# Kernel optimization log

Measured on AMD Instinct MI355X. Metric: run time of the kernel, lower is better.

## Reference

```python
import jax, jax.numpy as jnp
import numpy as np

B, S, E, H = 8, 1024, 1024, 16
D = E // H  # head dimension = 64


def setup_inputs() -> dict:
    key = jax.random.key(0)
    ks = jax.random.split(key, 9)
    sc = 1.0 / np.sqrt(E)
    return {
        "q": jax.random.normal(ks[0], (B, S, E), dtype=jnp.float32),
        "Wq_w": jax.random.normal(ks[1], (E, E), dtype=jnp.float32) * sc,
        "Wq_b": jax.random.normal(ks[2], (E,), dtype=jnp.float32) * 0.01,
        "Wk_w": jax.random.normal(ks[3], (E, E), dtype=jnp.float32) * sc,
        "Wk_b": jax.random.normal(ks[4], (E,), dtype=jnp.float32) * 0.01,
        "Wv_w": jax.random.normal(ks[5], (E, E), dtype=jnp.float32) * sc,
        "Wv_b": jax.random.normal(ks[6], (E,), dtype=jnp.float32) * 0.01,
        "Wo_w": jax.random.normal(ks[7], (E, E), dtype=jnp.float32) * sc,
        "Wo_b": jax.random.normal(ks[8], (E,), dtype=jnp.float32) * 0.01,
    }


def reference(q, Wq_w, Wq_b, Wk_w, Wk_b, Wv_w, Wv_b, Wo_w, Wo_b):
    # Linear projections (torch Linear: x @ W.T + b)
    Q = q @ Wq_w.T + Wq_b
    K = q @ Wk_w.T + Wk_b  # self-attention: k = v = q
    V = q @ Wv_w.T + Wv_b
    # [B, S, E] -> [B, H, S, D]
    Q = Q.reshape(B, S, H, D).transpose(0, 2, 1, 3)
    K = K.reshape(B, S, H, D).transpose(0, 2, 1, 3)
    V = V.reshape(B, S, H, D).transpose(0, 2, 1, 3)
    # Scores [B, H, S, S], scaled by sqrt(head_dim)
    scores = jnp.einsum('bhqd,bhkd->bhqk', Q, K) / jnp.sqrt(jnp.float32(D))
    attn = jax.nn.softmax(scores, axis=-1)
    # dropout p=0.0 (eval mode) -> identity
    out = jnp.einsum('bhqk,bhkd->bhqd', attn, V)
    out = out.transpose(0, 2, 1, 3).reshape(B, S, E)
    out = out @ Wo_w.T + Wo_b
    return out, attn
```

## Files before the change

### kernel.cpp

```cpp
#include <hip/hip_runtime.h>

using bf16x8 = __attribute__((ext_vector_type(8))) __bf16;
using f32x4  = __attribute__((ext_vector_type(4))) float;

#define NE 1024
#define C1E 0.18033688011112042f
#define C2E -11.541560327111707f

__device__ __forceinline__ unsigned short f2b(float f) {
    unsigned u = __builtin_bit_cast(unsigned, f);
    u = (u + 0x7FFFu + ((u >> 16) & 1u)) >> 16;
    return (unsigned short)u;
}

typedef __attribute__((address_space(1))) const void gvoid_t;
typedef __attribute__((address_space(3))) void lvoid_t;


__device__ __forceinline__ void stage128(const unsigned short* gbase, char* lds, int tid)
{
    const int w = tid >> 6, l = tid & 63;
    #pragma unroll
    for (int i = 0; i < 4; ++i) {
        int grp = i * 4 + w;
        int row = grp * 8 + (l >> 3);
        int srcb = ((l & 7) * 16) ^ ((l >> 3) << 4);
        const char* g = (const char*)(gbase + (size_t)row * NE) + srcb;
        __builtin_amdgcn_global_load_lds((gvoid_t*)g, (lvoid_t*)(lds + grp * 1024), 16, 0, 0);
    }
}

__device__ __forceinline__ void stage64x128(const unsigned short* gbase, char* lds, int tid)
{
    const int w = tid >> 6, l = tid & 63;
    #pragma unroll
    for (int i = 0; i < 2; ++i) {
        int grp = i * 4 + w;
        int row = grp * 8 + (l >> 3);
        int srcb = ((l & 7) * 16) ^ ((l >> 3) << 4);
        const char* g = (const char*)(gbase + (size_t)row * NE) + srcb;
        __builtin_amdgcn_global_load_lds((gvoid_t*)g, (lvoid_t*)(lds + grp * 1024), 16, 0, 0);
    }
}

__device__ __forceinline__ void stage64x256(const unsigned short* gbase, char* lds, int tid)
{
    const int w = tid >> 6, l = tid & 63;
    #pragma unroll
    for (int i = 0; i < 4; ++i) {
        int row0 = i * 16 + w * 4;
        int row = row0 + (l >> 4);
        int srcb = ((l & 15) * 16) ^ ((row & 7) << 4);
        const char* g = (const char*)(gbase + (size_t)row * 1024) + srcb;
        __builtin_amdgcn_global_load_lds((gvoid_t*)g, (lvoid_t*)(lds + row0 * 256), 16, 0, 0);
    }
}

__global__ __launch_bounds__(256)
void conv_bf16(const float* __restrict__ src, unsigned short* __restrict__ dst)
{
    size_t i = ((size_t)blockIdx.x * 256 + threadIdx.x) * 8;
    float4 a0 = *(const float4*)(src + i);
    float4 a1 = *(const float4*)(src + i + 4);
    uint4 p;
    p.x = f2b(a0.x) | ((unsigned)f2b(a0.y) << 16);
    p.y = f2b(a0.z) | ((unsigned)f2b(a0.w) << 16);
    p.z = f2b(a1.x) | ((unsigned)f2b(a1.y) << 16);
    p.w = f2b(a1.z) | ((unsigned)f2b(a1.w) << 16);
    *(uint4*)(dst + i) = p;
}

__global__ __launch_bounds__(256)
void conv_all(const float* __restrict__ q, const float* __restrict__ w0,
              const float* __restrict__ w1, const float* __restrict__ w2,
              unsigned short* __restrict__ qd, unsigned short* __restrict__ d0,
              unsigned short* __restrict__ d1, unsigned short* __restrict__ d2)
{
    int bid = blockIdx.x;
    const float* s; unsigned short* d; size_t off;
    if (bid < 4096) { s = q; d = qd; off = (size_t)bid * 2048; }
    else {
        int seg = (bid - 4096) >> 9, r = (bid - 4096) & 511;
        s = seg == 0 ? w0 : (seg == 1 ? w1 : w2);
        d = seg == 0 ? d0 : (seg == 1 ? d1 : d2);
        off = (size_t)r * 2048;
    }
    size_t i = off + threadIdx.x * 8;
    float4 a0 = *(const float4*)(s + i);
    float4 a1 = *(const float4*)(s + i + 4);
    uint4 p;
    p.x = f2b(a0.x) | ((unsigned)f2b(a0.y) << 16);
    p.y = f2b(a0.z) | ((unsigned)f2b(a0.w) << 16);
    p.z = f2b(a1.x) | ((unsigned)f2b(a1.y) << 16);
    p.w = f2b(a1.z) | ((unsigned)f2b(a1.w) << 16);
    *(uint4*)(d + i) = p;
}

__global__ __launch_bounds__(256, 2)
void qkv_proj(const unsigned short* __restrict__ A,
              const unsigned short* __restrict__ Wq, const unsigned short* __restrict__ Wk,
              const unsigned short* __restrict__ Wv,
              const float* __restrict__ bq, const float* __restrict__ bk,
              const float* __restrict__ bv,
              unsigned short* __restrict__ Qo, unsigned short* __restrict__ Ko,
              unsigned short* __restrict__ Vo)
{
    __shared__ char Asm[16384];
    __shared__ char Bsm[3][8192];
    const int tid  = threadIdx.x;
    const int lane = tid & 63;
    const int w    = tid >> 6;
    const int swz = (blockIdx.x & 7) * 128 + (blockIdx.x >> 3);
    const int rowbase = (swz >> 4) * 128;
    const int colbase = (swz & 15) * 64;
    f32x4 acc[3][2][4] = {};

    for (int kt = 0; kt < 16; ++kt) {
        __syncthreads();
        stage128(A + (size_t)rowbase * NE + kt * 64, Asm, tid);
        stage64x128(Wq + (size_t)colbase * NE + kt * 64, Bsm[0], tid);
        stage64x128(Wk + (size_t)colbase * NE + kt * 64, Bsm[1], tid);
        stage64x128(Wv + (size_t)colbase * NE + kt * 64, Bsm[2], tid);
        __syncthreads();
        #pragma unroll
        for (int ks = 0; ks < 2; ++ks) {
            const int kb = ks * 64 + (lane >> 4) * 16;
            bf16x8 af[2], bf[3][4];
            #pragma unroll
            for (int m = 0; m < 2; ++m) {
                int row = w * 32 + m * 16 + (lane & 15);
                af[m] = *(const bf16x8*)(Asm + ((row * 128 + kb) ^ ((row & 7) << 4)));
            }
            #pragma unroll
            for (int j = 0; j < 3; ++j)
                #pragma unroll
                for (int n = 0; n < 4; ++n) {
                    int row = n * 16 + (lane & 15);
                    bf[j][n] = *(const bf16x8*)(Bsm[j] + ((row * 128 + kb) ^ ((row & 7) << 4)));
                }
            #pragma unroll
            for (int j = 0; j < 3; ++j)
                #pragma unroll
                for (int m = 0; m < 2; ++m)
                    #pragma unroll
                    for (int n = 0; n < 4; ++n)
                        acc[j][m][n] = __builtin_amdgcn_mfma_f32_16x16x32_bf16(af[m], bf[j][n], acc[j][m][n], 0, 0, 0);
        }
    }

    #pragma unroll
    for (int m = 0; m < 2; ++m)
        #pragma unroll
        for (int n = 0; n < 4; ++n) {
            int col = colbase + n * 16 + (lane & 15);
            float bvq = bq[col], bvk = bk[col], bvv = bv[col];
            #pragma unroll
            for (int r = 0; r < 4; ++r) {
                int row = rowbase + w * 32 + m * 16 + (lane >> 4) * 4 + r;
                Qo[(size_t)row * NE + col] = f2b(acc[0][m][n][r] + bvq);
                Ko[(size_t)row * NE + col] = f2b(acc[1][m][n][r] + bvk);
                int b = row >> 10, s = row & 1023, h = col >> 6, d = col & 63;
                Vo[((size_t)((b * 16 + h) * 64 + d) << 10) + s] = f2b(acc[2][m][n][r] + bvv);
            }
        }
}

__global__ __launch_bounds__(256)
void proj_o(const unsigned short* __restrict__ A, const unsigned short* __restrict__ W,
            const float* __restrict__ bias, float* __restrict__ outp)
{
    __shared__ char Asm[16384], Bsm[16384];
    const int tid  = threadIdx.x;
    const int lane = tid & 63;
    const int wid  = tid >> 6;
    const int wr = wid >> 1, wc = wid & 1;
    const int swz = (blockIdx.x & 7) * 64 + (blockIdx.x >> 3);
    const int rowbase = (swz >> 3) * 128;
    const int colbase = (swz & 7) * 128;
    f32x4 acc[4][4] = {};

    for (int kt = 0; kt < 16; ++kt) {
        __syncthreads();
        stage128(A + (size_t)rowbase * NE + kt * 64, Asm, tid);
        stage128(W + (size_t)colbase * NE + kt * 64, Bsm, tid);
        __syncthreads();
        #pragma unroll
        for (int ks = 0; ks < 2; ++ks) {
            const int kb = ks * 64 + (lane >> 4) * 16;
            bf16x8 af[4], bf[4];
            #pragma unroll
            for (int m = 0; m < 4; ++m) {
                int row = wr * 64 + m * 16 + (lane & 15);
                af[m] = *(const bf16x8*)(Asm + ((row * 128 + kb) ^ ((row & 7) << 4)));
            }
            #pragma unroll
            for (int n = 0; n < 4; ++n) {
                int row = wc * 64 + n * 16 + (lane & 15);
                bf[n] = *(const bf16x8*)(Bsm + ((row * 128 + kb) ^ ((row & 7) << 4)));
            }
            #pragma unroll
            for (int m = 0; m < 4; ++m)
                #pragma unroll
                for (int n = 0; n < 4; ++n)
                    acc[m][n] = __builtin_amdgcn_mfma_f32_16x16x32_bf16(af[m], bf[n], acc[m][n], 0, 0, 0);
        }
    }

    #pragma unroll
    for (int m = 0; m < 4; ++m)
        #pragma unroll
        for (int n = 0; n < 4; ++n) {
            int col = colbase + wc * 64 + n * 16 + (lane & 15);
            float bv = bias[col];
            #pragma unroll
            for (int r = 0; r < 4; ++r) {
                int row = rowbase + wr * 64 + m * 16 + (lane >> 4) * 4 + r;
                outp[(size_t)row * NE + col] = acc[m][n][r] + bv;
            }
        }
}

__global__ __launch_bounds__(256, 2)
void fused_attn(const unsigned short* __restrict__ Q,
                const unsigned short* __restrict__ K,
                const unsigned short* __restrict__ VT,
                float* __restrict__ attn, unsigned short* __restrict__ Og)
{
    __shared__ char Ksm[16384];
    __shared__ char Vsm[16384];
    __shared__ char Psm[32768];
    __shared__ float rs4[4][128];
    __shared__ float lt[128];
    const int tid  = threadIdx.x;
    const int lane = tid & 63;
    const int w    = tid >> 6;
    const int swzb = (blockIdx.x & 7) * 128 + (blockIdx.x >> 3);
    const int bh = swzb >> 3, qt = swzb & 7;
    const int b = bh >> 4, h = bh & 15;
    const unsigned short* Qg = Q  + (size_t)(b * 1024 + qt * 128) * 1024 + h * 64;
    const unsigned short* Kg = K  + (size_t)(b * 1024) * 1024 + h * 64;
    const unsigned short* Vg = VT + (size_t)bh * 64 * 1024;

    stage128(Qg, Psm, tid);
    __syncthreads();
    bf16x8 qf[2][8];
    #pragma unroll
    for (int ks = 0; ks < 2; ++ks) {
        const int kb = ks * 64 + (lane >> 4) * 16;
        #pragma unroll
        for (int n = 0; n < 8; ++n) {
            int row = n * 16 + (lane & 15);
            qf[ks][n] = *(const bf16x8*)(Psm + ((row * 128 + kb) ^ ((row & 7) << 4)));
        }
    }
    stage128(Kg, Ksm, tid);

    float rs_p[8] = {0.f, 0.f, 0.f, 0.f, 0.f, 0.f, 0.f, 0.f};
    for (int kt = 0; kt < 8; ++kt) {
        __syncthreads();
        f32x4 sa[2][8] = {};
        __builtin_amdgcn_s_setprio(1);
        #pragma unroll
        for (int ks = 0; ks < 2; ++ks) {
            const int kb = ks * 64 + (lane >> 4) * 16;
            bf16x8 kf[2];
            #pragma unroll
            for (int m = 0; m < 2; ++m) {
                int row = w * 32 + m * 16 + (lane & 15);
                kf[m] = *(const bf16x8*)(Ksm + ((row * 128 + kb) ^ ((row & 7) << 4)));
            }
            #pragma unroll
            for (int m = 0; m < 2; ++m)
                #pragma unroll
                for (int n = 0; n < 8; ++n)
                    sa[m][n] = __builtin_amdgcn_mfma_f32_16x16x32_bf16(kf[m], qf[ks][n], sa[m][n], 0, 0, 0);
        }
        __builtin_amdgcn_s_setprio(0);
        __syncthreads();
        if (kt < 7) stage128(Kg + (size_t)((kt + 1) * 128) * 1024, Ksm, tid);
        #pragma unroll
        for (int n = 0; n < 8; ++n)
            #pragma unroll
            for (int m = 0; m < 2; ++m)
                #pragma unroll
                for (int r = 0; r < 4; ++r)
                    rs_p[n] += exp2f(fmaf(sa[m][n][r], C1E, C2E));
    }
    #pragma unroll
    for (int n = 0; n < 8; ++n) {
        rs_p[n] += __shfl_xor(rs_p[n], 16);
        rs_p[n] += __shfl_xor(rs_p[n], 32);
    }
    if (lane < 16) {
        #pragma unroll
        for (int n = 0; n < 8; ++n) rs4[w][n * 16 + lane] = rs_p[n];
    }
    __syncthreads();
    if (tid < 128) {
        float l = rs4[0][tid] + rs4[1][tid] + rs4[2][tid] + rs4[3][tid];
        lt[tid] = C2E - __log2f(l);
    }
    stage128(Kg, Ksm, tid);

    f32x4 oa[2][4] = {};
    float* attnq = attn + ((size_t)bh * 1024 + qt * 128) * 1024;
    for (int kt = 0; kt < 8; ++kt) {
        __syncthreads();
        stage64x256(Vg + kt * 128, Vsm, tid);
        f32x4 sa[2][8] = {};
        __builtin_amdgcn_s_setprio(1);
        #pragma unroll
        for (int ks = 0; ks < 2; ++ks) {
            const int kb = ks * 64 + (lane >> 4) * 16;
            bf16x8 kf[2];
            #pragma unroll
            for (int m = 0; m < 2; ++m) {
                int row = w * 32 + m * 16 + (lane & 15);
                kf[m] = *(const bf16x8*)(Ksm + ((row * 128 + kb) ^ ((row & 7) << 4)));
            }
            #pragma unroll
            for (int m = 0; m < 2; ++m)
                #pragma unroll
                for (int n = 0; n < 8; ++n)
                    sa[m][n] = __builtin_amdgcn_mfma_f32_16x16x32_bf16(kf[m], qf[ks][n], sa[m][n], 0, 0, 0);
        }
        __builtin_amdgcn_s_setprio(0);
        #pragma unroll
        for (int n = 0; n < 8; ++n) {
            int q = n * 16 + (lane & 15);
            float ltq = lt[q];
            #pragma unroll
            for (int m = 0; m < 2; ++m) {
                int k0 = w * 32 + m * 16 + (lane >> 4) * 4;
                float4 p4;
                p4.x = exp2f(fmaf(sa[m][n][0], C1E, ltq));
                p4.y = exp2f(fmaf(sa[m][n][1], C1E, ltq));
                p4.z = exp2f(fmaf(sa[m][n][2], C1E, ltq));
                p4.w = exp2f(fmaf(sa[m][n][3], C1E, ltq));
                *(float4*)(attnq + (size_t)q * 1024 + kt * 128 + k0) = p4;
                uint2 pk;
                pk.x = f2b(p4.x) | ((unsigned)f2b(p4.y) << 16);
                pk.y = f2b(p4.z) | ((unsigned)f2b(p4.w) << 16);
                *(uint2*)(Psm + ((q * 256 + k0 * 2) ^ ((q & 7) << 4))) = pk;
            }
        }
        __syncthreads();
        if (kt < 7) stage128(Kg + (size_t)((kt + 1) * 128) * 1024, Ksm, tid);
        __builtin_amdgcn_s_setprio(1);
        #pragma unroll
        for (int ks = 0; ks < 4; ++ks) {
            const int kb = ks * 64 + (lane >> 4) * 16;
            bf16x8 pa[2], vb[4];
            #pragma unroll
            for (int m2 = 0; m2 < 2; ++m2) {
                int row = w * 32 + m2 * 16 + (lane & 15);
                pa[m2] = *(const bf16x8*)(Psm + ((row * 256 + kb) ^ ((row & 7) << 4)));
            }
            #pragma unroll
            for (int n2 = 0; n2 < 4; ++n2) {
                int d = n2 * 16 + (lane & 15);
                vb[n2] = *(const bf16x8*)(Vsm + d * 256 + (kb ^ ((d & 7) << 4)));
            }
            #pragma unroll
            for (int m2 = 0; m2 < 2; ++m2)
                #pragma unroll
                for (int n2 = 0; n2 < 4; ++n2)
                    oa[m2][n2] = __builtin_amdgcn_mfma_f32_16x16x32_bf16(pa[m2], vb[n2], oa[m2][n2], 0, 0, 0);
        }
        __builtin_amdgcn_s_setprio(0);
    }
    unsigned short* Ob = Og + (size_t)(b * 1024 + qt * 128) * 1024 + h * 64;
    #pragma unroll
    for (int m2 = 0; m2 < 2; ++m2)
        #pragma unroll
        for (int n2 = 0; n2 < 4; ++n2) {
            int d = n2 * 16 + (lane & 15);
            #pragma unroll
            for (int r = 0; r < 4; ++r) {
                int qrow = w * 32 + m2 * 16 + (lane >> 4) * 4 + r;
                Ob[(size_t)qrow * 1024 + d] = f2b(oa[m2][n2][r]);
            }
        }
}

extern "C" void kernel_launch(void* const* d_in, const int* in_sizes, int n_in,
                              void* d_out, int out_size, void* d_ws, size_t ws_size,
                              hipStream_t stream) {
    (void)in_sizes; (void)n_in; (void)out_size; (void)ws_size;
    const float* q    = (const float*)d_in[0];
    const float* Wq_w = (const float*)d_in[1];
    const float* Wq_b = (const float*)d_in[2];
    const float* Wk_w = (const float*)d_in[3];
    const float* Wk_b = (const float*)d_in[4];
    const float* Wv_w = (const float*)d_in[5];
    const float* Wv_b = (const float*)d_in[6];
    const float* Wo_w = (const float*)d_in[7];
    const float* Wo_b = (const float*)d_in[8];

    char* ws = (char*)d_ws;
    unsigned short* Qws  = (unsigned short*)(ws);
    unsigned short* Kws  = (unsigned short*)(ws + (16u << 20));
    unsigned short* VTws = (unsigned short*)(ws + (32u << 20));

    float* outp  = (float*)d_out;
    float* attnp = outp + 8388608;

    char* scr = (char*)attnp;
    unsigned short* qbf = (unsigned short*)scr;
    unsigned short* wqb = (unsigned short*)(scr + (16u << 20));
    unsigned short* wkb = (unsigned short*)(scr + (18u << 20));
    unsigned short* wvb = (unsigned short*)(scr + (20u << 20));

    dim3 blk(256);
    conv_all<<<dim3(4096 + 3 * 512), blk, 0, stream>>>(q, Wq_w, Wk_w, Wv_w, qbf, wqb, wkb, wvb);
    qkv_proj<<<dim3(1024), blk, 0, stream>>>(qbf, wqb, wkb, wvb, Wq_b, Wk_b, Wv_b, Qws, Kws, VTws);
    fused_attn<<<dim3(1024), blk, 0, stream>>>(Qws, Kws, VTws, attnp, Qws);
    conv_bf16<<<dim3(512), blk, 0, stream>>>(Wo_w, Kws);
    proj_o<<<dim3(512), blk, 0, stream>>>(Qws, Kws, Wo_b, outp);
}
```

Before: 278.0 us.

## Halve P tile LDS, double-buffer K in row-sum pass, raise occupancy to 3

Shrinks the P staging buffer from 32KB to 16KB by writing and consuming the probability tile in two 64-key halves, with extra barriers between halves. This allows launch bounds of 3 blocks per CU instead of 2. The first row-sum pass now double-buffers K tiles between Ksm and the freed Psm, removing one barrier per iteration and overlapping loads with MFMA work. It also swaps the manual bf16 rounding for native casts. The risks are more register pressure under the tighter bound and more synchronisation in the PV loop.

```diff
diff --git a/kernel.cpp b/kernel.cpp
--- a/kernel.cpp
+++ b/kernel.cpp
@@ -1,6 +1,7 @@
 #include <hip/hip_runtime.h>
 
 using bf16x8 = __attribute__((ext_vector_type(8))) __bf16;
+using bf16x4 = __attribute__((ext_vector_type(4))) __bf16;
 using f32x4  = __attribute__((ext_vector_type(4))) float;
 
 #define NE 1024
@@ -220,7 +221,7 @@
         }
 }
 
-__global__ __launch_bounds__(256, 2)
+__global__ __launch_bounds__(256, 3)
 void fused_attn(const unsigned short* __restrict__ Q,
                 const unsigned short* __restrict__ K,
                 const unsigned short* __restrict__ VT,
@@ -228,7 +229,7 @@
 {
     __shared__ char Ksm[16384];
     __shared__ char Vsm[16384];
-    __shared__ char Psm[32768];
+    __shared__ char Psm[16384];
     __shared__ float rs4[4][128];
     __shared__ float lt[128];
     const int tid  = threadIdx.x;
@@ -242,6 +243,7 @@
     const unsigned short* Vg = VT + (size_t)bh * 64 * 1024;
 
     stage128(Qg, Psm, tid);
+    stage128(Kg, Ksm, tid);
     __syncthreads();
     bf16x8 qf[2][8];
     #pragma unroll
@@ -253,11 +255,14 @@
             qf[ks][n] = *(const bf16x8*)(Psm + ((row * 128 + kb) ^ ((row & 7) << 4)));
         }
     }
-    stage128(Kg, Ksm, tid);
 
     float rs_p[8] = {0.f, 0.f, 0.f, 0.f, 0.f, 0.f, 0.f, 0.f};
+    #pragma unroll
     for (int kt = 0; kt < 8; ++kt) {
-        __syncthreads();
+        char* cur = (kt & 1) ? Psm : Ksm;
+        char* nxt = (kt & 1) ? Ksm : Psm;
+        __syncthreads();
+        stage128(Kg + (size_t)(((kt + 1) & 7) * 128) * 1024, nxt, tid);
         f32x4 sa[2][8] = {};
         __builtin_amdgcn_s_setprio(1);
         #pragma unroll
@@ -267,7 +272,7 @@
             #pragma unroll
             for (int m = 0; m < 2; ++m) {
                 int row = w * 32 + m * 16 + (lane & 15);
-                kf[m] = *(const bf16x8*)(Ksm + ((row * 128 + kb) ^ ((row & 7) << 4)));
+                kf[m] = *(const bf16x8*)(cur + ((row * 128 + kb) ^ ((row & 7) << 4)));
             }
             #pragma unroll
             for (int m = 0; m < 2; ++m)
@@ -276,8 +281,6 @@
                     sa[m][n] = __builtin_amdgcn_mfma_f32_16x16x32_bf16(kf[m], qf[ks][n], sa[m][n], 0, 0, 0);
         }
         __builtin_amdgcn_s_setprio(0);
-        __syncthreads();
-        if (kt < 7) stage128(Kg + (size_t)((kt + 1) * 128) * 1024, Ksm, tid);
         #pragma unroll
         for (int n = 0; n < 8; ++n)
             #pragma unroll
@@ -300,7 +303,6 @@
         float l = rs4[0][tid] + rs4[1][tid] + rs4[2][tid] + rs4[3][tid];
         lt[tid] = C2E - __log2f(l);
     }
-    stage128(Kg, Ksm, tid);
 
     f32x4 oa[2][4] = {};
     float* attnq = attn + ((size_t)bh * 1024 + qt * 128) * 1024;
@@ -338,36 +340,53 @@
                 p4.z = exp2f(fmaf(sa[m][n][2], C1E, ltq));
                 p4.w = exp2f(fmaf(sa[m][n][3], C1E, ltq));
                 *(float4*)(attnq + (size_t)q * 1024 + kt * 128 + k0) = p4;
-                uint2 pk;
-                pk.x = f2b(p4.x) | ((unsigned)f2b(p4.y) << 16);
-                pk.y = f2b(p4.z) | ((unsigned)f2b(p4.w) << 16);
-                *(uint2*)(Psm + ((q * 256 + k0 * 2) ^ ((q & 7) << 4))) = pk;
-            }
-        }
-        __syncthreads();
-        if (kt < 7) stage128(Kg + (size_t)((kt + 1) * 128) * 1024, Ksm, tid);
-        __builtin_amdgcn_s_setprio(1);
-        #pragma unroll
-        for (int ks = 0; ks < 4; ++ks) {
-            const int kb = ks * 64 + (lane >> 4) * 16;
-            bf16x8 pa[2], vb[4];
-            #pragma unroll
-            for (int m2 = 0; m2 < 2; ++m2) {
-                int row = w * 32 + m2 * 16 + (lane & 15);
-                pa[m2] = *(const bf16x8*)(Psm + ((row * 256 + kb) ^ ((row & 7) << 4)));
-            }
-            #pragma unroll
-            for (int n2 = 0; n2 < 4; ++n2) {
-                int d = n2 * 16 + (lane & 15);
-                vb[n2] = *(const bf16x8*)(Vsm + d * 256 + (kb ^ ((d & 7) << 4)));
-            }
-            #pragma unroll
-            for (int m2 = 0; m2 < 2; ++m2)
-                #pragma unroll
-                for (int n2 = 0; n2 < 4; ++n2)
-                    oa[m2][n2] = __builtin_amdgcn_mfma_f32_16x16x32_bf16(pa[m2], vb[n2], oa[m2][n2], 0, 0, 0);
-        }
-        __builtin_amdgcn_s_setprio(0);
+                sa[m][n][0] = p4.x; sa[m][n][1] = p4.y;
+                sa[m][n][2] = p4.z; sa[m][n][3] = p4.w;
+            }
+        }
+        #pragma unroll
+        for (int hh = 0; hh < 2; ++hh) {
+            if ((w >> 1) == hh) {
+                #pragma unroll
+                for (int n = 0; n < 8; ++n) {
+                    int q = n * 16 + (lane & 15);
+                    #pragma unroll
+                    for (int m = 0; m < 2; ++m) {
+                        int kh = (w * 32 + m * 16 + (lane >> 4) * 4) & 63;
+                        bf16x4 pb;
+                        pb[0] = (__bf16)sa[m][n][0]; pb[1] = (__bf16)sa[m][n][1];
+                        pb[2] = (__bf16)sa[m][n][2]; pb[3] = (__bf16)sa[m][n][3];
+                        *(bf16x4*)(Psm + ((q * 128 + kh * 2) ^ ((q & 7) << 4))) = pb;
+                    }
+                }
+            }
+            __syncthreads();
+            if (hh == 0 && kt < 7) stage128(Kg + (size_t)((kt + 1) * 128) * 1024, Ksm, tid);
+            __builtin_amdgcn_s_setprio(1);
+            #pragma unroll
+            for (int ks2 = 0; ks2 < 2; ++ks2) {
+                const int kbp = ks2 * 64 + (lane >> 4) * 16;
+                const int kbv = hh * 128 + kbp;
+                bf16x8 pa[2], vb[4];
+                #pragma unroll
+                for (int m2 = 0; m2 < 2; ++m2) {
+                    int row = w * 32 + m2 * 16 + (lane & 15);
+                    pa[m2] = *(const bf16x8*)(Psm + ((row * 128 + kbp) ^ ((row & 7) << 4)));
+                }
+                #pragma unroll
+                for (int n2 = 0; n2 < 4; ++n2) {
+                    int d = n2 * 16 + (lane & 15);
+                    vb[n2] = *(const bf16x8*)(Vsm + d * 256 + (kbv ^ ((d & 7) << 4)));
+                }
+                #pragma unroll
+                for (int m2 = 0; m2 < 2; ++m2)
+                    #pragma unroll
+                    for (int n2 = 0; n2 < 4; ++n2)
+                        oa[m2][n2] = __builtin_amdgcn_mfma_f32_16x16x32_bf16(pa[m2], vb[n2], oa[m2][n2], 0, 0, 0);
+            }
+            __builtin_amdgcn_s_setprio(0);
+            if (hh == 0) __syncthreads();
+        }
     }
     unsigned short* Ob = Og + (size_t)(b * 1024 + qt * 128) * 1024 + h * 64;
     #pragma unroll
@@ -378,7 +397,7 @@
             #pragma unroll
             for (int r = 0; r < 4; ++r) {
                 int qrow = w * 32 + m2 * 16 + (lane >> 4) * 4 + r;
-                Ob[(size_t)qrow * 1024 + d] = f2b(oa[m2][n2][r]);
+                Ob[(size_t)qrow * 1024 + d] = __builtin_bit_cast(unsigned short, (__bf16)oa[m2][n2][r]);
             }
         }
 }
```

New measurement: 522.7 us. +88.0%, slower.
